# Performance work log

Measured on AMD Instinct MI355X. Metric: run time of the kernel, lower is better.

## Reference

```python
import jax, jax.numpy as jnp
import numpy as np

B, V, C, D = 32, 64, 32, 256
VOCAB = 20000
NUM_T = 1000


def _run_lstm(x, Wih, Whh, b):
    # x: [T, B, H_in]; torch-style single-layer LSTM with zero initial state
    T, Bb, _ = x.shape
    H = Whh.shape[1]
    def step(carry, xt):
        h, c = carry
        z = xt @ Wih.T + h @ Whh.T + b
        i, f, g, o = jnp.split(z, 4, axis=-1)
        c = jax.nn.sigmoid(f) * c + jax.nn.sigmoid(i) * jnp.tanh(g)
        h = jax.nn.sigmoid(o) * jnp.tanh(c)
        return (h, c), h
    h0 = jnp.zeros((Bb, H), x.dtype)
    _, ys = jax.lax.scan(step, (h0, h0), x)
    return ys


def _forward(input_seqs, masks, lengths, seq_time_step, code_masks, emb, WQ1, WK1,
             decay, initial, lstm_Wih, lstm_Whh, lstm_b, hs_Wih, hs_Whh, hs_b,
             whk_W, whk_b, w1_W, w1_b, w2_W, w2_b, fuse_W, fuse_b, lab_W, lab_b,
             betas, Wdiff, diffusion_time_t, normal_noise):
    Bb, Vv, Cc = input_seqs.shape
    tok = input_seqs.reshape(-1, Cc)                      # [B*V, C]
    x = emb[tok]                                          # [B*V, C, D]
    q = x @ WQ1.T
    k = x @ WK1.T
    dp = jnp.einsum('bcd,bed->bce', q, k)                 # [B*V, C, C]
    cm = code_masks.reshape(-1, Cc)
    dp = dp - cm[:, None, :] - cm[:, :, None]
    sp = jax.nn.softmax(dp / jnp.sqrt(jnp.float32(D)), axis=-1)
    femb = jnp.einsum('bce,bed->bcd', sp, x)              # attended code embeddings
    femb = ((cm - 1e20) / -1e20)[:, :, None] * femb       # zero out padded codes
    dec = decay[tok][..., None]                           # [B*V, C, 1]
    ini = initial[tok][..., None]
    t = seq_time_step.reshape(-1)[:, None, None]          # [B*V, 1, 1]
    gate = jax.nn.sigmoid(dec * t + ini)                  # time-decay gate
    vv = jnp.einsum('bcx,bcd->bd', gate, femb)            # [B*V, D] visit vector
    vv = vv.reshape(Bb, Vv, -1).transpose(1, 0, 2)        # [V, B, D]

    lstm_out = _run_lstm(vv, lstm_Wih, lstm_Whh, lstm_b)  # [V, B, D]
    t_lstm = lstm_out.transpose(1, 0, 2)                  # [B, V, D]
    hiddenstate = _run_lstm(lstm_out, hs_Wih, hs_Whh, hs_b).transpose(1, 0, 2)

    # Vectorized form of the original per-step python loop.
    # NOTE: the original always uses e_k = t_lstm_out[:, 0:1, :] (step 0) -- kept faithfully.
    e_k = t_lstm[:, 0:1, :]                               # [B, 1, D]
    whp = hiddenstate[:, :-1, :] @ whk_W.T + whk_b        # [B, V-1, D]
    cat = jnp.concatenate([jnp.broadcast_to(e_k, whp.shape), whp], axis=-1)
    attn = jax.nn.softmax(jnp.tanh(cat @ w1_W.T + w1_b) @ w2_W.T + w2_b, axis=-1)
    rest = e_k * attn[..., 0:1] + whp * attn[..., 1:2]
    aligned = jnp.concatenate([e_k, rest], axis=1)        # [B, V, D]

    alpha = jnp.cumprod(1.0 - betas)[diffusion_time_t][:, None, None]
    noisy = aligned * jnp.sqrt(alpha) + normal_noise * jnp.sqrt(1.0 - alpha)
    predicted_noise = noisy @ Wdiff                       # surrogate for UNetModel (source not provided)
    gen = aligned + (normal_noise - predicted_noise)

    fused = jnp.concatenate([t_lstm, gen], axis=-1) @ fuse_W.T + fuse_b   # [B, V, D]
    mask_final = (jnp.arange(Vv)[None, :] == (lengths - 1)[:, None]).astype(fused.dtype)
    final = (fused * mask_final[:, :, None]).sum(axis=1)  # select last valid visit
    return final @ lab_W.T + lab_b                        # [B, 2]


def setup_inputs() -> dict:
    key = jax.random.key(0)
    ks = jax.random.split(key, 20)
    s = 0.05
    n = lambda i, shp: jax.random.normal(ks[i], shp, jnp.float32) * s
    emb = jax.random.normal(ks[0], (VOCAB + 1, D), jnp.float32) * 0.02
    emb = emb.at[VOCAB].set(0.0)  # padding_idx row
    return {
        'input_seqs': jax.random.randint(ks[1], (B, V, C), 0, VOCAB),
        'masks': jnp.zeros((B, V), jnp.float32),
        'lengths': jax.random.randint(ks[2], (B,), 1, V + 1),
        'seq_time_step': jax.random.uniform(ks[3], (B, V), jnp.float32),
        'code_masks': jnp.zeros((B, V, C), jnp.float32),
        'emb': emb,
        'WQ1': n(4, (D, D)), 'WK1': n(5, (D, D)),
        'decay': jnp.full((VOCAB + 1,), -0.1, jnp.float32),
        'initial': jnp.full((VOCAB + 1,), 1.0, jnp.float32),
        'lstm_Wih': n(6, (4 * D, D)), 'lstm_Whh': n(7, (4 * D, D)),
        'lstm_b': jnp.zeros((4 * D,), jnp.float32),
        'hs_Wih': n(8, (4 * D, D)), 'hs_Whh': n(9, (4 * D, D)),
        'hs_b': jnp.zeros((4 * D,), jnp.float32),
        'whk_W': n(10, (D, D)), 'whk_b': jnp.zeros((D,), jnp.float32),
        'w1_W': n(11, (64, 2 * D)), 'w1_b': jnp.zeros((64,), jnp.float32),
        'w2_W': n(12, (2, 64)), 'w2_b': jnp.zeros((2,), jnp.float32),
        'fuse_W': n(13, (D, 2 * D)), 'fuse_b': jnp.zeros((D,), jnp.float32),
        'lab_W': n(14, (2, D)), 'lab_b': jnp.zeros((2,), jnp.float32),
        'betas': jnp.linspace(1e-4, 0.02, NUM_T, dtype=jnp.float32),
        'Wdiff': n(15, (D, D)),
        'diffusion_time_t': jax.random.randint(ks[16], (B,), 0, NUM_T),
        'normal_noise': jax.random.normal(ks[17], (B, V, D), jnp.float32),
    }


def reference(input_seqs, masks, lengths, seq_time_step, code_masks, emb, WQ1, WK1,
              decay, initial, lstm_Wih, lstm_Whh, lstm_b, hs_Wih, hs_Whh, hs_b,
              whk_W, whk_b, w1_W, w1_b, w2_W, w2_b, fuse_W, fuse_b, lab_W, lab_b,
              betas, Wdiff, diffusion_time_t, normal_noise):
    return _forward(input_seqs, masks, lengths, seq_time_step, code_masks, emb, WQ1, WK1,
                    decay, initial, lstm_Wih, lstm_Whh, lstm_b, hs_Wih, hs_Whh, hs_b,
                    whk_W, whk_b, w1_W, w1_b, w2_W, w2_b, fuse_W, fuse_b, lab_W, lab_b,
                    betas, Wdiff, diffusion_time_t, normal_noise)
```

## Files before the change

### kernel.cpp

```cpp
#include <hip/hip_runtime.h>
#include <hip/hip_bf16.h>
#include <cmath>

typedef __attribute__((ext_vector_type(8))) short bf16x8;
typedef __attribute__((ext_vector_type(4))) float f32x4;
typedef __attribute__((ext_vector_type(4))) int i32x4;
typedef __attribute__((ext_vector_type(2))) unsigned int u32x2;

__device__ __forceinline__ float bf2f(unsigned short u) {
    unsigned int x = ((unsigned int)u) << 16;
    return __builtin_bit_cast(float, x);
}
__device__ __forceinline__ unsigned short f2bf(float f) {
    unsigned int x = __builtin_bit_cast(unsigned int, f);
    unsigned int lsb = (x >> 16) & 1u;
    x += 0x7fffu + lsb;
    return (unsigned short)(x >> 16);
}
__device__ __forceinline__ float sigm(float z) {
    return 1.f / (1.f + __expf(-z));
}
__device__ __forceinline__ float rcpf(float x) { return __builtin_amdgcn_rcpf(x); }
__device__ __forceinline__ float sigm_f(float z) { return rcpf(1.f + __expf(-z)); }
__device__ __forceinline__ float tanh_f(float z) { return 1.f - 2.f * rcpf(1.f + __expf(2.f * z)); }

__device__ __forceinline__ long ldg_sc8l(const void* p) {
    long r;
    asm volatile("global_load_dwordx2 %0, %1, off sc1" : "=v"(r) : "v"(p) : "memory");
    return r;
}
__device__ __forceinline__ u32x2 ldg_sc_u2(const void* p) {
    u32x2 r;
    asm volatile("global_load_dwordx2 %0, %1, off sc1" : "=v"(r) : "v"(p) : "memory");
    return r;
}
__device__ __forceinline__ void stg_sc_u2(void* p, u32x2 v) {
    asm volatile("global_store_dwordx2 %0, %1, off sc1" :: "v"(p), "v"(v) : "memory");
}

__global__ void __launch_bounds__(256) pack_all(
    const float* __restrict__ Whh1, const float* __restrict__ Wih2,
    const float* __restrict__ Whh2, const float* __restrict__ Wih1,
    const float* __restrict__ WQ1, const float* __restrict__ WK1,
    const float* __restrict__ betas, const int* __restrict__ dift,
    const float* __restrict__ whk_W, const float* __restrict__ fuse_W,
    const float* __restrict__ w1_W,
    long* __restrict__ Wq, float* __restrict__ cs,
    unsigned short* __restrict__ W1h, unsigned short* __restrict__ M_pk,
    float* __restrict__ alpha, int* __restrict__ flags,
    float* __restrict__ whkT, float* __restrict__ fuseT,
    float* __restrict__ w1T) {
    int blk = blockIdx.x, tid = threadIdx.x;
    if (blk < 384) {
        int R = blk * 8 + (tid >> 5);
        int mat = R >> 10;
        int n = R & 1023;
        int t32 = tid & 31;
        const float* src = (mat == 0) ? Whh1 : (mat == 1 ? Wih2 : Whh2);
        const float* rp = src + (size_t)n * 256 + t32 * 8;
        float v[8];
        float mx = 0.f;
        for (int j = 0; j < 8; ++j) { v[j] = rp[j]; mx = fmaxf(mx, fabsf(v[j])); }
        for (int m = 1; m <= 16; m <<= 1) mx = fmaxf(mx, __shfl_xor(mx, m));
        float inv = mx > 0.f ? 127.f / mx : 0.f;
        unsigned int lo = 0, hi = 0;
        for (int j = 0; j < 4; ++j) {
            int iv = __float2int_rn(v[j] * inv);
            lo |= ((unsigned int)(unsigned char)(signed char)iv) << (8 * j);
            int iv2 = __float2int_rn(v[4 + j] * inv);
            hi |= ((unsigned int)(unsigned char)(signed char)iv2) << (8 * j);
        }
        int g = n >> 8, rem = n & 255;
        int w8 = rem >> 5, dt = (rem >> 4) & 1, cc = rem & 15;
        int t8 = g * 2 + dt;
        int kb = t32 >> 2, q = t32 & 3;
        unsigned int* dst = (unsigned int*)Wq +
            ((size_t)((mat * 512 + w8 * 64 + t8 * 8 + kb) * 64) + q * 16 + cc) * 2;
        dst[0] = lo;
        dst[1] = hi;
        if (t32 == 0) cs[mat * 1024 + n] = mx / 16129.f;
    } else if (blk < 512) {
        int cch = (blk - 384) * 256 + tid;
        int nt = cch >> 9;
        int r = cch & 511;
        int kb = r >> 6;
        int lane = r & 63;
        int grow = nt * 16 + (lane & 15);
        int k0 = kb * 32 + (lane >> 4) * 8;
        const float* sp = Wih1 + (size_t)grow * 256 + k0;
        bf16x8 hi;
        for (int j = 0; j < 8; ++j) hi[j] = (short)f2bf(sp[j]);
        *reinterpret_cast<bf16x8*>(W1h + (size_t)cch * 8) = hi;
    } else if (blk == 512) {
        if (tid < 32) {
            int tb = dift[tid];
            float p = 1.f;
            for (int i = 0; i <= tb; ++i) p *= (1.f - betas[i]);
            alpha[tid] = p;
        }
    } else if (blk == 513) {
        for (int i = tid; i < 4096; i += 256) flags[i] = 0;
    } else if (blk < 578) {
        int gid = (blk - 514) * 256 + tid;
        for (int i = 0; i < 4; ++i) {
            int e = gid + i * 16384;
            int k = e >> 8, dd = e & 255;
            whkT[e] = whk_W[(size_t)dd * 256 + k];
        }
    } else if (blk < 706) {
        int gid = (blk - 578) * 256 + tid;
        for (int i = 0; i < 4; ++i) {
            int e = gid + i * 32768;
            int k = e >> 8, dd = e & 255;
            fuseT[e] = fuse_W[(size_t)dd * 512 + k];
        }
    } else if (blk < 738) {
        int gid = (blk - 706) * 256 + tid;
        for (int i = 0; i < 4; ++i) {
            int e = gid + i * 8192;
            int k = e >> 6, j = e & 63;
            w1T[e] = w1_W[(size_t)j * 512 + k];
        }
    } else {
        __shared__ unsigned short As[256][32];
        __shared__ unsigned short Bs[256][32];
        int bx = blk - 738;
        int e0 = (bx >> 3) << 5;
        int f0 = (bx & 7) << 5;
        int col = tid & 31, rr = tid >> 5;
        for (int rep = 0; rep < 32; ++rep) {
            int d = rep * 8 + rr;
            As[d][col] = f2bf(WQ1[d * 256 + e0 + col]);
            Bs[d][col] = f2bf(WK1[d * 256 + f0 + col]);
        }
        __syncthreads();
        int el = tid & 31;
        int fl0 = tid >> 5;
        for (int i = 0; i < 4; ++i) {
            int fl = fl0 + 8 * i;
            float acc = 0.f;
            for (int d = 0; d < 256; ++d)
                acc += bf2f(As[d][el]) * bf2f(Bs[d][fl]);
            int e = e0 + el, f = f0 + fl;
            int kb = e >> 5, r = (e >> 3) & 3, j = e & 7;
            int nb = f >> 4;
            int lane = (r << 4) | (f & 15);
            M_pk[(((nb * 8 + kb) * 64) + lane) * 8 + j] = f2bf(acc);
        }
    }
}

__global__ void __launch_bounds__(256) eprep(const float* __restrict__ emb,
                                             const unsigned short* __restrict__ M_pk,
                                             unsigned short* __restrict__ Ep) {
    __shared__ __align__(16) unsigned short x_bf[32 * 256];
    int v0 = blockIdx.x * 32;
    int tid = threadIdx.x;
    for (int it = 0; it < 8; ++it) {
        int fidx = it * 256 + tid;
        int cc = fidx >> 6;
        int f4 = fidx & 63;
        int row = v0 + cc;
        float4 vx = make_float4(0.f, 0.f, 0.f, 0.f);
        if (row < 20001)
            vx = *(reinterpret_cast<const float4*>(emb + (size_t)row * 256) + f4);
        int colx = f4 * 4;
        ushort4 w;
        w.x = f2bf(vx.x); w.y = f2bf(vx.y); w.z = f2bf(vx.z); w.w = f2bf(vx.w);
        *reinterpret_cast<ushort4*>(&x_bf[cc * 256 + (colx ^ ((cc & 7) << 3))]) = w;
    }
    __syncthreads();
    int wv = tid >> 6, lane = tid & 63, lr = lane & 15, lk = lane >> 4;
    f32x4 acc[2][4];
    for (int a = 0; a < 2; ++a)
        for (int n = 0; n < 4; ++n) acc[a][n] = (f32x4){0.f, 0.f, 0.f, 0.f};
    for (int kb = 0; kb < 8; ++kb) {
        bf16x8 afr[2];
        for (int mb = 0; mb < 2; ++mb) {
            int row = mb * 16 + lr;
            int colx = kb * 32 + lk * 8;
            afr[mb] = *reinterpret_cast<const bf16x8*>(&x_bf[row * 256 + (colx ^ ((row & 7) << 3))]);
        }
        for (int nbi = 0; nbi < 4; ++nbi) {
            int nb = wv * 4 + nbi;
            bf16x8 bfr = *reinterpret_cast<const bf16x8*>(M_pk + (((nb * 8 + kb) * 64) + lane) * 8);
            acc[0][nbi] = __builtin_amdgcn_mfma_f32_16x16x32_bf16(afr[0], bfr, acc[0][nbi], 0, 0, 0);
            acc[1][nbi] = __builtin_amdgcn_mfma_f32_16x16x32_bf16(afr[1], bfr, acc[1][nbi], 0, 0, 0);
        }
    }
    for (int mb = 0; mb < 2; ++mb)
        for (int nbi = 0; nbi < 4; ++nbi)
            for (int r = 0; r < 4; ++r) {
                int row = mb * 16 + lk * 4 + r;
                int col = wv * 64 + nbi * 16 + lr;
                if (v0 + row < 20001)
                    Ep[(size_t)(v0 + row) * 256 + col] = f2bf(acc[mb][nbi][r]);
            }
}

__global__ void __launch_bounds__(256) attn_bags(
    const int* __restrict__ seqs, const float* __restrict__ tstep,
    const float* __restrict__ cmask, const float* __restrict__ emb,
    const float* __restrict__ decay, const float* __restrict__ initial,
    const unsigned short* __restrict__ Ep, float* __restrict__ vv) {
    __shared__ __align__(16) unsigned short x_bf[32 * 256];
    __shared__ __align__(16) unsigned short t1_bf[32 * 256];
    __shared__ float dp_f[32 * 33];
    __shared__ float gate_sh[32];
    __shared__ float cm_sh[32];
    __shared__ int tok_sh[32];
    __shared__ float w_sh[32];

    int bag = blockIdx.x;
    int tid = threadIdx.x;

    if (tid < 32) {
        int tok = seqs[bag * 32 + tid];
        tok_sh[tid] = tok;
        float cm = cmask[bag * 32 + tid];
        cm_sh[tid] = cm;
        float tt = tstep[bag];
        float g = sigm(decay[tok] * tt + initial[tok]);
        g *= (cm - 1e20f) / (-1e20f);
        gate_sh[tid] = g;
    }
    __syncthreads();

    for (int it = 0; it < 8; ++it) {
        int fidx = it * 256 + tid;
        int c = fidx >> 6;
        int f4 = fidx & 63;
        const float4* src = reinterpret_cast<const float4*>(emb + (size_t)tok_sh[c] * 256) + f4;
        float4 vx = *src;
        int colx = f4 * 4;
        int eidx = c * 256 + (colx ^ ((c & 7) << 3));
        ushort4 w;
        w.x = f2bf(vx.x); w.y = f2bf(vx.y); w.z = f2bf(vx.z); w.w = f2bf(vx.w);
        *reinterpret_cast<ushort4*>(&x_bf[eidx]) = w;
    }
    for (int it = 0; it < 4; ++it) {
        int idx = it * 256 + tid;
        int cc = idx >> 5;
        int colx = (idx & 31) * 8;
        bf16x8 e = *reinterpret_cast<const bf16x8*>(Ep + (size_t)tok_sh[cc] * 256 + colx);
        *reinterpret_cast<bf16x8*>(&t1_bf[cc * 256 + (colx ^ ((cc & 7) << 3))]) = e;
    }
    __syncthreads();

    int wv = tid >> 6;
    int lane = tid & 63;
    int lr = lane & 15;
    int lk = lane >> 4;

    {
        int mb = wv >> 1, nb2 = wv & 1;
        f32x4 dacc = (f32x4){0.f, 0.f, 0.f, 0.f};
        for (int kb = 0; kb < 8; ++kb) {
            int cola = kb * 32 + lk * 8;
            int rowa = mb * 16 + lr;
            bf16x8 afr = *reinterpret_cast<const bf16x8*>(&t1_bf[rowa * 256 + (cola ^ ((rowa & 7) << 3))]);
            int rowb = nb2 * 16 + lr;
            bf16x8 bfr = *reinterpret_cast<const bf16x8*>(&x_bf[rowb * 256 + (cola ^ ((rowb & 7) << 3))]);
            dacc = __builtin_amdgcn_mfma_f32_16x16x32_bf16(afr, bfr, dacc, 0, 0, 0);
        }
        for (int r = 0; r < 4; ++r) {
            int c = mb * 16 + lk * 4 + r;
            int e = nb2 * 16 + lr;
            dp_f[c * 33 + e] = dacc[r];
        }
    }
    __syncthreads();

    if (tid < 32) {
        int c = tid;
        float cmc = cm_sh[c];
        float lg[32];
        float mx = -1e30f;
        for (int e = 0; e < 32; ++e) {
            float l = (dp_f[c * 33 + e] - cmc - cm_sh[e]) * 0.0625f;
            lg[e] = l;
            mx = fmaxf(mx, l);
        }
        float s = 0.f;
        for (int e = 0; e < 32; ++e) { float ex = __expf(lg[e] - mx); lg[e] = ex; s += ex; }
        float inv = 1.f / s;
        for (int e = 0; e < 32; ++e) dp_f[c * 33 + e] = lg[e] * inv;
    }
    __syncthreads();
    if (tid < 32) {
        int e = tid;
        float a2 = 0.f;
        for (int c = 0; c < 32; ++c) a2 += gate_sh[c] * dp_f[c * 33 + e];
        w_sh[e] = a2;
    }
    __syncthreads();

    float accv = 0.f;
    int d = tid;
    for (int e = 0; e < 32; ++e)
        accv += w_sh[e] * bf2f(x_bf[e * 256 + (d ^ ((e & 7) << 3))]);
    vv[(size_t)bag * 256 + d] = accv;
}

__global__ void __launch_bounds__(256) x1_mfma(const float* __restrict__ vv,
                                               const unsigned short* __restrict__ W1h,
                                               const float* __restrict__ lstm_b,
                                               unsigned short* __restrict__ X1bf) {
    __shared__ __align__(16) unsigned short xs[32 * 256];
    int blk = blockIdx.x;
    int rb = blk >> 3, gb = blk & 7;
    int tid = threadIdx.x;
    for (int it = 0; it < 8; ++it) {
        int idx = it * 256 + tid;
        int row = idx >> 6, f4 = idx & 63;
        float4 v = *reinterpret_cast<const float4*>(vv + (size_t)(rb * 32 + row) * 256 + f4 * 4);
        ushort4 w;
        w.x = f2bf(v.x); w.y = f2bf(v.y); w.z = f2bf(v.z); w.w = f2bf(v.w);
        *reinterpret_cast<ushort4*>(&xs[row * 256 + ((f4 * 4) ^ ((row & 7) << 3))]) = w;
    }
    __syncthreads();
    int wv = tid >> 6, lane = tid & 63, cl = lane & 15, kh = lane >> 4;
    f32x4 acc[2][2];
    for (int n = 0; n < 2; ++n) {
        int nt = gb * 8 + wv * 2 + n;
        float bz = lstm_b[nt * 16 + cl];
        acc[n][0] = (f32x4){bz, bz, bz, bz};
        acc[n][1] = (f32x4){bz, bz, bz, bz};
    }
    #pragma unroll
    for (int kb = 0; kb < 8; ++kb) {
        int k = kb * 32 + kh * 8;
        bf16x8 a0 = *reinterpret_cast<const bf16x8*>(&xs[cl * 256 + (k ^ ((cl & 7) << 3))]);
        bf16x8 a1 = *reinterpret_cast<const bf16x8*>(&xs[(16 + cl) * 256 + (k ^ (((16 + cl) & 7) << 3))]);
        for (int n = 0; n < 2; ++n) {
            int nt = gb * 8 + wv * 2 + n;
            size_t o = ((size_t)(nt * 8 + kb) * 64 + lane) * 8;
            bf16x8 bh = *reinterpret_cast<const bf16x8*>(W1h + o);
            acc[n][0] = __builtin_amdgcn_mfma_f32_16x16x32_bf16(a0, bh, acc[n][0], 0, 0, 0);
            acc[n][1] = __builtin_amdgcn_mfma_f32_16x16x32_bf16(a1, bh, acc[n][1], 0, 0, 0);
        }
    }
    for (int n = 0; n < 2; ++n) {
        int nt = gb * 8 + wv * 2 + n;
        int g = nt * 16 + cl;
        int dX = g & 255, gt = g >> 8;
        for (int mt = 0; mt < 2; ++mt)
            for (int r = 0; r < 4; ++r) {
                int row = rb * 32 + mt * 16 + kh * 4 + r;
                int b = row >> 6, t = row & 63;
                X1bf[((size_t)t * 32 + b) * 1024 + dX * 4 + gt] = f2bf(acc[n][mt][r]);
            }
    }
}

__global__ void __launch_bounds__(512, 2) lstm_persist(
    const long* __restrict__ Wq, const float* __restrict__ cs,
    const unsigned short* __restrict__ X1bf, const float* __restrict__ hs_b,
    unsigned short* __restrict__ h1bf, unsigned short* __restrict__ h2bf,
    signed char* h1q, unsigned short* p1, int* flags) {
    int role = blockIdx.x;
    int half = role & 1;
    int kind = role >> 1;
    int tid = threadIdx.x;
    int w = tid >> 6, lane = tid & 63, c = lane & 15, q = lane >> 4;

    long wt[64];
    #pragma unroll
    for (int t8 = 0; t8 < 8; ++t8)
        #pragma unroll
        for (int kb = 0; kb < 8; ++kb)
            wt[t8 * 8 + kb] = Wq[(size_t)((kind * 512 + w * 64 + t8 * 8 + kb) * 64) + lane];
    float csv[8];
    #pragma unroll
    for (int t8 = 0; t8 < 8; ++t8) {
        int g = t8 >> 1, dt = t8 & 1;
        csv[t8] = cs[kind * 1024 + g * 256 + w * 32 + dt * 16 + c];
    }

    if (kind == 0) {
        __shared__ signed char hq[2][16][272];
        float cstate[8] = {0.f, 0.f, 0.f, 0.f, 0.f, 0.f, 0.f, 0.f};
        int B0 = half * 16 + q * 4;
        int dbase = w * 32;
        for (int t = 0; t < 64; ++t) {
            ushort4 xv[8];
            #pragma unroll
            for (int dt = 0; dt < 2; ++dt)
                #pragma unroll
                for (int r = 0; r < 4; ++r)
                    xv[dt * 4 + r] = *reinterpret_cast<const ushort4*>(
                        X1bf + ((size_t)(t * 32 + B0 + r) * 1024 + (dbase + dt * 16 + c) * 4));
            i32x4 acc[8];
            #pragma unroll
            for (int i = 0; i < 8; ++i) acc[i] = (i32x4){0, 0, 0, 0};
            if (t > 0) {
                int pb = (t - 1) & 1;
                long a[8];
                #pragma unroll
                for (int kb = 0; kb < 8; ++kb)
                    a[kb] = *reinterpret_cast<const long*>(&hq[pb][c][kb * 32 + q * 8]);
                #pragma unroll
                for (int t8 = 0; t8 < 8; ++t8)
                    #pragma unroll
                    for (int kb = 0; kb < 8; ++kb)
                        acc[t8] = __builtin_amdgcn_mfma_i32_16x16x32_i8(
                            a[kb], wt[t8 * 8 + kb], acc[t8], 0, 0, 0);
            }
            float hnv[8];
            unsigned int hvb[8];
            #pragma unroll
            for (int dt = 0; dt < 2; ++dt)
                #pragma unroll
                for (int r = 0; r < 4; ++r) {
                    int idx = dt * 4 + r;
                    ushort4 x = xv[idx];
                    float zi = (float)acc[0 + dt][r] * csv[0 + dt] + bf2f(x.x);
                    float zf = (float)acc[2 + dt][r] * csv[2 + dt] + bf2f(x.y);
                    float zg = (float)acc[4 + dt][r] * csv[4 + dt] + bf2f(x.z);
                    float zo = (float)acc[6 + dt][r] * csv[6 + dt] + bf2f(x.w);
                    float cn = sigm_f(zf) * cstate[idx] + sigm_f(zi) * tanh_f(zg);
                    float hn = sigm_f(zo) * tanh_f(cn);
                    cstate[idx] = cn;
                    hnv[idx] = hn;
                    int hv = __float2int_rn(hn * 127.f);
                    hq[t & 1][q * 4 + r][dbase + dt * 16 + c] = (signed char)hv;
                    hvb[idx] = (unsigned int)(unsigned char)(signed char)hv;
                }
            #pragma unroll
            for (int dt = 0; dt < 2; ++dt)
                #pragma unroll
                for (int r = 0; r < 4; ++r) {
                    unsigned int b = hvb[dt * 4 + r];
                    unsigned int p = (unsigned int)__shfl_xor((int)b, 1);
                    unsigned int pair = (c & 1) ? (p | (b << 8)) : (b | (p << 8));
                    unsigned int pq = (unsigned int)__shfl_xor((int)pair, 2);
                    unsigned int quad = (c & 2) ? (pq | (pair << 16)) : (pair | (pq << 16));
                    unsigned int oh = (unsigned int)__shfl_xor((int)quad, 4);
                    if ((c & 7) == 0) {
                        u32x2 v8;
                        v8.x = quad; v8.y = oh;
                        stg_sc_u2(h1q + (size_t)(t * 32 + B0 + r) * 256 + dbase + dt * 16 + c, v8);
                    }
                }
            #pragma unroll
            for (int dt = 0; dt < 2; ++dt)
                #pragma unroll
                for (int r = 0; r < 4; ++r) {
                    unsigned int ph = f2bf(hnv[dt * 4 + r]);
                    unsigned int pp = (unsigned int)__shfl_xor((int)ph, 1);
                    if (!(c & 1))
                        *reinterpret_cast<unsigned int*>(
                            h1bf + (size_t)(t * 32 + B0 + r) * 256 + dbase + dt * 16 + c) =
                            ph | (pp << 16);
                }
            __syncthreads();
            if (tid == 0)
                __hip_atomic_store(flags + (t * 2 + half) * 16, 1,
                                   __ATOMIC_RELAXED, __HIP_MEMORY_SCOPE_AGENT);
        }
    } else if (kind == 1) {
        for (int s2 = 0; s2 < 64; s2 += 2) {
            const int* fp = flags + ((s2 + 1) * 2 + half) * 16;
            while (__hip_atomic_load(fp, __ATOMIC_RELAXED, __HIP_MEMORY_SCOPE_AGENT) == 0)
                __builtin_amdgcn_s_sleep(1);
            __builtin_amdgcn_sched_barrier(0);
            const signed char* hb0 = h1q + (size_t)(s2 * 32 + half * 16) * 256;
            const signed char* hb1 = h1q + (size_t)((s2 + 1) * 32 + half * 16) * 256;
            long a[8], b[8];
            #pragma unroll
            for (int kb = 0; kb < 8; ++kb) {
                a[kb] = ldg_sc8l(hb0 + c * 256 + kb * 32 + q * 8);
                b[kb] = ldg_sc8l(hb1 + c * 256 + kb * 32 + q * 8);
            }
            asm volatile("s_waitcnt vmcnt(0)" ::: "memory");
            __builtin_amdgcn_sched_barrier(0);
            #pragma unroll
            for (int step = 0; step < 2; ++step) {
                int s = s2 + step;
                i32x4 acc[8];
                #pragma unroll
                for (int i = 0; i < 8; ++i) acc[i] = (i32x4){0, 0, 0, 0};
                #pragma unroll
                for (int t8 = 0; t8 < 8; ++t8)
                    #pragma unroll
                    for (int kb = 0; kb < 8; ++kb)
                        acc[t8] = __builtin_amdgcn_mfma_i32_16x16x32_i8(
                            step ? b[kb] : a[kb], wt[t8 * 8 + kb], acc[t8], 0, 0, 0);
                #pragma unroll
                for (int t8 = 0; t8 < 8; ++t8) {
                    int g = t8 >> 1, dt = t8 & 1;
                    int n = g * 256 + w * 32 + dt * 16 + c;
                    u32x2 pv;
                    pv.x = (unsigned int)f2bf((float)acc[t8][0] * csv[t8]) |
                           ((unsigned int)f2bf((float)acc[t8][1] * csv[t8]) << 16);
                    pv.y = (unsigned int)f2bf((float)acc[t8][2] * csv[t8]) |
                           ((unsigned int)f2bf((float)acc[t8][3] * csv[t8]) << 16);
                    stg_sc_u2(p1 + ((size_t)(s * 2 + half) * 1024 + n) * 16 + q * 4, pv);
                }
            }
            __syncthreads();
            if (tid == 0)
                __hip_atomic_store(flags + 2048 + ((s2 >> 1) * 2 + half) * 16, 1,
                                   __ATOMIC_RELAXED, __HIP_MEMORY_SCOPE_AGENT);
        }
    } else {
        __shared__ signed char hq2[2][16][272];
        float cstate[8] = {0.f, 0.f, 0.f, 0.f, 0.f, 0.f, 0.f, 0.f};
        float bias[8];
        #pragma unroll
        for (int t8 = 0; t8 < 8; ++t8) {
            int g = t8 >> 1, dt = t8 & 1;
            bias[t8] = hs_b[g * 256 + w * 32 + dt * 16 + c];
        }
        int B0 = half * 16 + q * 4;
        int dbase = w * 32;
        for (int s = 0; s < 64; ++s) {
            if ((s & 1) == 0) {
                const int* fp = flags + 2048 + ((s >> 1) * 2 + half) * 16;
                while (__hip_atomic_load(fp, __ATOMIC_RELAXED, __HIP_MEMORY_SCOPE_AGENT) == 0)
                    __builtin_amdgcn_s_sleep(1);
                __builtin_amdgcn_sched_barrier(0);
            }
            u32x2 pv[8];
            #pragma unroll
            for (int t8 = 0; t8 < 8; ++t8) {
                int g = t8 >> 1, dt = t8 & 1;
                int n = g * 256 + w * 32 + dt * 16 + c;
                pv[t8] = ldg_sc_u2(p1 + ((size_t)(s * 2 + half) * 1024 + n) * 16 + q * 4);
            }
            i32x4 acc[8];
            #pragma unroll
            for (int i = 0; i < 8; ++i) acc[i] = (i32x4){0, 0, 0, 0};
            if (s > 0) {
                int pb = (s - 1) & 1;
                long a[8];
                #pragma unroll
                for (int kb = 0; kb < 8; ++kb)
                    a[kb] = *reinterpret_cast<const long*>(&hq2[pb][c][kb * 32 + q * 8]);
                asm volatile("s_waitcnt vmcnt(0)" ::: "memory");
                __builtin_amdgcn_sched_barrier(0);
                #pragma unroll
                for (int t8 = 0; t8 < 8; ++t8)
                    #pragma unroll
                    for (int kb = 0; kb < 8; ++kb)
                        acc[t8] = __builtin_amdgcn_mfma_i32_16x16x32_i8(
                            a[kb], wt[t8 * 8 + kb], acc[t8], 0, 0, 0);
            } else {
                asm volatile("s_waitcnt vmcnt(0)" ::: "memory");
                __builtin_amdgcn_sched_barrier(0);
            }
            float hnv[8];
            #pragma unroll
            for (int dt = 0; dt < 2; ++dt)
                #pragma unroll
                for (int r = 0; r < 4; ++r) {
                    int idx = dt * 4 + r;
                    float p_i = bf2f((unsigned short)((r < 2 ? pv[0 + dt].x : pv[0 + dt].y) >> ((r & 1) * 16)));
                    float p_f = bf2f((unsigned short)((r < 2 ? pv[2 + dt].x : pv[2 + dt].y) >> ((r & 1) * 16)));
                    float p_g = bf2f((unsigned short)((r < 2 ? pv[4 + dt].x : pv[4 + dt].y) >> ((r & 1) * 16)));
                    float p_o = bf2f((unsigned short)((r < 2 ? pv[6 + dt].x : pv[6 + dt].y) >> ((r & 1) * 16)));
                    float zi = (float)acc[0 + dt][r] * csv[0 + dt] + p_i + bias[0 + dt];
                    float zf = (float)acc[2 + dt][r] * csv[2 + dt] + p_f + bias[2 + dt];
                    float zg = (float)acc[4 + dt][r] * csv[4 + dt] + p_g + bias[4 + dt];
                    float zo = (float)acc[6 + dt][r] * csv[6 + dt] + p_o + bias[6 + dt];
                    float cn = sigm_f(zf) * cstate[idx] + sigm_f(zi) * tanh_f(zg);
                    float hn = sigm_f(zo) * tanh_f(cn);
                    cstate[idx] = cn;
                    hnv[idx] = hn;
                    hq2[s & 1][q * 4 + r][dbase + dt * 16 + c] = (signed char)__float2int_rn(hn * 127.f);
                }
            #pragma unroll
            for (int dt = 0; dt < 2; ++dt)
                #pragma unroll
                for (int r = 0; r < 4; ++r) {
                    unsigned int ph = f2bf(hnv[dt * 4 + r]);
                    unsigned int pp = (unsigned int)__shfl_xor((int)ph, 1);
                    if (!(c & 1))
                        *reinterpret_cast<unsigned int*>(
                            h2bf + (size_t)(s * 32 + B0 + r) * 256 + dbase + dt * 16 + c) =
                            ph | (pp << 16);
                }
            __syncthreads();
        }
    }
}

__global__ void __launch_bounds__(256) tail_k(
    const int* __restrict__ lengths,
    const unsigned short* __restrict__ h1, const unsigned short* __restrict__ h2,
    const float* __restrict__ whkT, const float* __restrict__ whk_b,
    const float* __restrict__ w1T, const float* __restrict__ w1_b,
    const float* __restrict__ w2_W, const float* __restrict__ w2_b,
    const float* __restrict__ fuseT, const float* __restrict__ fuse_b,
    const float* __restrict__ lab_W, const float* __restrict__ lab_b,
    const float* __restrict__ Wdiff, const float* __restrict__ alpha,
    const float* __restrict__ noise, float* __restrict__ out) {
    __shared__ float ek[256], tv[256], hs[256], whp[256], a1s[64];
    __shared__ float noisy_s[256], fin[512], fused_s[256], attn_s[2];
    int b = blockIdx.x, tid = threadIdx.x;
    int vstar = lengths[b] - 1;
    {
        ek[tid] = bf2f(h1[(size_t)b * 256 + tid]);
        tv[tid] = bf2f(h1[((size_t)vstar * 32 + b) * 256 + tid]);
        if (vstar > 0)
            hs[tid] = bf2f(h2[((size_t)(vstar - 1) * 32 + b) * 256 + tid]);
    }
    __syncthreads();

    float aligned;
    if (vstar > 0) {
        float s0 = 0.f, s1 = 0.f, s2 = 0.f, s3 = 0.f;
        for (int k = 0; k < 256; k += 4) {
            s0 += whkT[(k + 0) * 256 + tid] * hs[k + 0];
            s1 += whkT[(k + 1) * 256 + tid] * hs[k + 1];
            s2 += whkT[(k + 2) * 256 + tid] * hs[k + 2];
            s3 += whkT[(k + 3) * 256 + tid] * hs[k + 3];
        }
        whp[tid] = whk_b[tid] + s0 + s1 + s2 + s3;
        __syncthreads();
        if (tid < 64) {
            float a0 = 0.f, a1 = 0.f, a2 = 0.f, a3 = 0.f;
            for (int k = 0; k < 256; k += 4) {
                a0 += w1T[(k + 0) * 64 + tid] * ek[k + 0];
                a1 += w1T[(k + 1) * 64 + tid] * ek[k + 1];
                a2 += w1T[(k + 2) * 64 + tid] * ek[k + 2];
                a3 += w1T[(k + 3) * 64 + tid] * ek[k + 3];
            }
            for (int k = 0; k < 256; k += 4) {
                a0 += w1T[(256 + k + 0) * 64 + tid] * whp[k + 0];
                a1 += w1T[(256 + k + 1) * 64 + tid] * whp[k + 1];
                a2 += w1T[(256 + k + 2) * 64 + tid] * whp[k + 2];
                a3 += w1T[(256 + k + 3) * 64 + tid] * whp[k + 3];
            }
            a1s[tid] = tanhf(w1_b[tid] + a0 + a1 + a2 + a3);
        }
        __syncthreads();
        if (tid < 2) {
            float a3 = w2_b[tid];
            const float* wr2 = w2_W + tid * 64;
            for (int k = 0; k < 64; ++k) a3 += wr2[k] * a1s[k];
            attn_s[tid] = a3;
        }
        __syncthreads();
        float m = fmaxf(attn_s[0], attn_s[1]);
        float e0 = __expf(attn_s[0] - m), e1 = __expf(attn_s[1] - m);
        float inv = 1.f / (e0 + e1);
        aligned = ek[tid] * (e0 * inv) + whp[tid] * (e1 * inv);
    } else {
        aligned = ek[tid];
    }

    float al = alpha[b];
    float sa = sqrtf(al), sb = sqrtf(1.f - al);
    float nz = noise[((size_t)b * 64 + vstar) * 256 + tid];
    noisy_s[tid] = aligned * sa + nz * sb;
    __syncthreads();
    {
        float p0 = 0.f, p1v = 0.f, p2 = 0.f, p3 = 0.f;
        for (int k = 0; k < 256; k += 4) {
            p0 += noisy_s[k + 0] * Wdiff[(size_t)(k + 0) * 256 + tid];
            p1v += noisy_s[k + 1] * Wdiff[(size_t)(k + 1) * 256 + tid];
            p2 += noisy_s[k + 2] * Wdiff[(size_t)(k + 2) * 256 + tid];
            p3 += noisy_s[k + 3] * Wdiff[(size_t)(k + 3) * 256 + tid];
        }
        float gen = aligned + nz - (p0 + p1v + p2 + p3);
        fin[tid] = tv[tid];
        fin[256 + tid] = gen;
    }
    __syncthreads();
    {
        float f0 = 0.f, f1 = 0.f, f2 = 0.f, f3 = 0.f;
        for (int k = 0; k < 512; k += 4) {
            f0 += fuseT[(k + 0) * 256 + tid] * fin[k + 0];
            f1 += fuseT[(k + 1) * 256 + tid] * fin[k + 1];
            f2 += fuseT[(k + 2) * 256 + tid] * fin[k + 2];
            f3 += fuseT[(k + 3) * 256 + tid] * fin[k + 3];
        }
        fused_s[tid] = fuse_b[tid] + f0 + f1 + f2 + f3;
    }
    __syncthreads();
    if (tid < 2) {
        float o = lab_b[tid];
        const float* lw = lab_W + tid * 256;
        for (int k = 0; k < 256; ++k) o += lw[k] * fused_s[k];
        out[b * 2 + tid] = o;
    }
}

extern "C" void kernel_launch(void* const* d_in, const int* in_sizes, int n_in,
                              void* d_out, int out_size, void* d_ws, size_t ws_size,
                              hipStream_t stream) {
    const int*   seqs    = (const int*)  d_in[0];
    const int*   lengths = (const int*)  d_in[2];
    const float* tstep   = (const float*)d_in[3];
    const float* cmask   = (const float*)d_in[4];
    const float* emb     = (const float*)d_in[5];
    const float* WQ1     = (const float*)d_in[6];
    const float* WK1     = (const float*)d_in[7];
    const float* decay   = (const float*)d_in[8];
    const float* initial = (const float*)d_in[9];
    const float* Wih1    = (const float*)d_in[10];
    const float* Whh1    = (const float*)d_in[11];
    const float* lstm_b  = (const float*)d_in[12];
    const float* Wih2    = (const float*)d_in[13];
    const float* Whh2    = (const float*)d_in[14];
    const float* hs_b    = (const float*)d_in[15];
    const float* whk_W   = (const float*)d_in[16];
    const float* whk_b   = (const float*)d_in[17];
    const float* w1_W    = (const float*)d_in[18];
    const float* w1_b    = (const float*)d_in[19];
    const float* w2_W    = (const float*)d_in[20];
    const float* w2_b    = (const float*)d_in[21];
    const float* fuse_W  = (const float*)d_in[22];
    const float* fuse_b  = (const float*)d_in[23];
    const float* lab_W   = (const float*)d_in[24];
    const float* lab_b   = (const float*)d_in[25];
    const float* betas   = (const float*)d_in[26];
    const float* Wdiff   = (const float*)d_in[27];
    const int*   dift    = (const int*)  d_in[28];
    const float* noise   = (const float*)d_in[29];
    float* out = (float*)d_out;

    float* ws = (float*)d_ws;
    size_t off = 0;
    auto alloc = [&](size_t nfloats) { size_t r = off; off += (nfloats + 63) & ~(size_t)63; return r; };
    unsigned short* M_pk  = (unsigned short*)(ws + alloc(32768));
    float*          alpha = ws + alloc(64);
    float*          cs    = ws + alloc(3072);
    int*            flags = (int*)(ws + alloc(4096));
    float*          vv    = ws + alloc(524288);
    unsigned short* X1bf  = (unsigned short*)(ws + alloc(1048576));
    unsigned short* h1bf  = (unsigned short*)(ws + alloc(262144));
    unsigned short* h2bf  = (unsigned short*)(ws + alloc(262144));
    unsigned short* p1    = (unsigned short*)(ws + alloc(1048576));
    long*           Wq    = (long*)(ws + alloc(196608));
    unsigned short* W1h   = (unsigned short*)(ws + alloc(131072));
    float*          whkT  = ws + alloc(65536);
    float*          fuseT = ws + alloc(131072);
    float*          w1T   = ws + alloc(32768);
    signed char*    h1q   = (signed char*)(ws + alloc(131072));
    unsigned short* Ep    = (unsigned short*)(ws + alloc(2560128));

    pack_all<<<802, 256, 0, stream>>>(Whh1, Wih2, Whh2, Wih1, WQ1, WK1, betas, dift,
                                      whk_W, fuse_W, w1_W,
                                      Wq, cs, W1h, M_pk, alpha, flags,
                                      whkT, fuseT, w1T);
    eprep<<<626, 256, 0, stream>>>(emb, M_pk, Ep);
    attn_bags<<<2048, 256, 0, stream>>>(seqs, tstep, cmask, emb, decay, initial, Ep, vv);
    x1_mfma<<<512, 256, 0, stream>>>(vv, W1h, lstm_b, X1bf);
    lstm_persist<<<6, 512, 0, stream>>>(Wq, cs, X1bf, hs_b, h1bf, h2bf, h1q, p1, flags);
    tail_k<<<32, 256, 0, stream>>>(lengths, h1bf, h2bf, whkT, whk_b,
                                   w1T, w1_b, w2_W, w2_b, fuseT, fuse_b,
                                   lab_W, lab_b, Wdiff, alpha, noise, out);
}
```

Baseline: 373.4 us.

## Split LSTM recurrence over 16 waves per block and pipeline projection per step

The persistent LSTM kernel now launches 1024 threads (16 waves) per role block instead of 512, so each wave owns 16 hidden units and 32 MFMAs per step instead of 32 units and 64. This halves per-wave register-resident weights and the serial MFMA chain on the recurrent critical path. The projection role also changes from batching two timesteps per flag wait to signalling every step, which lets the second LSTM start sooner. The cost is more flag polling traffic and more waves contending for the same CU's MFMA units.

Result: slower. 441.1 us (+18.2%).

```diff
diff --git a/kernel.cpp b/kernel.cpp
--- a/kernel.cpp
+++ b/kernel.cpp
@@ -353,7 +353,7 @@
     }
 }
 
-__global__ void __launch_bounds__(512, 2) lstm_persist(
+__global__ void __launch_bounds__(1024, 4) lstm_persist(
     const long* __restrict__ Wq, const float* __restrict__ cs,
     const unsigned short* __restrict__ X1bf, const float* __restrict__ hs_b,
     unsigned short* __restrict__ h1bf, unsigned short* __restrict__ h2bf,
@@ -362,37 +362,33 @@
     int half = role & 1;
     int kind = role >> 1;
     int tid = threadIdx.x;
-    int w = tid >> 6, lane = tid & 63, c = lane & 15, q = lane >> 4;
-
-    long wt[64];
+    int w = tid >> 6;
+    int lane = tid & 63, c = lane & 15, q = lane >> 4;
+    int d = w * 16 + c;
+
+    long wt[4][8];
     #pragma unroll
-    for (int t8 = 0; t8 < 8; ++t8)
+    for (int g = 0; g < 4; ++g)
         #pragma unroll
         for (int kb = 0; kb < 8; ++kb)
-            wt[t8 * 8 + kb] = Wq[(size_t)((kind * 512 + w * 64 + t8 * 8 + kb) * 64) + lane];
-    float csv[8];
+            wt[g][kb] = Wq[(size_t)((kind * 512 + (w >> 1) * 64 + (g * 2 + (w & 1)) * 8 + kb) * 64) + lane];
+    float csv[4];
     #pragma unroll
-    for (int t8 = 0; t8 < 8; ++t8) {
-        int g = t8 >> 1, dt = t8 & 1;
-        csv[t8] = cs[kind * 1024 + g * 256 + w * 32 + dt * 16 + c];
-    }
+    for (int g = 0; g < 4; ++g) csv[g] = cs[kind * 1024 + g * 256 + d];
 
     if (kind == 0) {
         __shared__ signed char hq[2][16][272];
-        float cstate[8] = {0.f, 0.f, 0.f, 0.f, 0.f, 0.f, 0.f, 0.f};
+        float cstate[4] = {0.f, 0.f, 0.f, 0.f};
         int B0 = half * 16 + q * 4;
-        int dbase = w * 32;
         for (int t = 0; t < 64; ++t) {
-            ushort4 xv[8];
-            #pragma unroll
-            for (int dt = 0; dt < 2; ++dt)
-                #pragma unroll
-                for (int r = 0; r < 4; ++r)
-                    xv[dt * 4 + r] = *reinterpret_cast<const ushort4*>(
-                        X1bf + ((size_t)(t * 32 + B0 + r) * 1024 + (dbase + dt * 16 + c) * 4));
-            i32x4 acc[8];
-            #pragma unroll
-            for (int i = 0; i < 8; ++i) acc[i] = (i32x4){0, 0, 0, 0};
+            ushort4 xv[4];
+            #pragma unroll
+            for (int r = 0; r < 4; ++r)
+                xv[r] = *reinterpret_cast<const ushort4*>(
+                    X1bf + ((size_t)(t * 32 + B0 + r) * 1024 + d * 4));
+            i32x4 acc[4];
+            #pragma unroll
+            for (int g = 0; g < 4; ++g) acc[g] = (i32x4){0, 0, 0, 0};
             if (t > 0) {
                 int pb = (t - 1) & 1;
                 long a[8];
@@ -400,137 +396,112 @@
                 for (int kb = 0; kb < 8; ++kb)
                     a[kb] = *reinterpret_cast<const long*>(&hq[pb][c][kb * 32 + q * 8]);
                 #pragma unroll
-                for (int t8 = 0; t8 < 8; ++t8)
+                for (int g = 0; g < 4; ++g)
                     #pragma unroll
                     for (int kb = 0; kb < 8; ++kb)
-                        acc[t8] = __builtin_amdgcn_mfma_i32_16x16x32_i8(
-                            a[kb], wt[t8 * 8 + kb], acc[t8], 0, 0, 0);
-            }
-            float hnv[8];
-            unsigned int hvb[8];
-            #pragma unroll
-            for (int dt = 0; dt < 2; ++dt)
-                #pragma unroll
-                for (int r = 0; r < 4; ++r) {
-                    int idx = dt * 4 + r;
-                    ushort4 x = xv[idx];
-                    float zi = (float)acc[0 + dt][r] * csv[0 + dt] + bf2f(x.x);
-                    float zf = (float)acc[2 + dt][r] * csv[2 + dt] + bf2f(x.y);
-                    float zg = (float)acc[4 + dt][r] * csv[4 + dt] + bf2f(x.z);
-                    float zo = (float)acc[6 + dt][r] * csv[6 + dt] + bf2f(x.w);
-                    float cn = sigm_f(zf) * cstate[idx] + sigm_f(zi) * tanh_f(zg);
-                    float hn = sigm_f(zo) * tanh_f(cn);
-                    cstate[idx] = cn;
-                    hnv[idx] = hn;
-                    int hv = __float2int_rn(hn * 127.f);
-                    hq[t & 1][q * 4 + r][dbase + dt * 16 + c] = (signed char)hv;
-                    hvb[idx] = (unsigned int)(unsigned char)(signed char)hv;
+                        acc[g] = __builtin_amdgcn_mfma_i32_16x16x32_i8(
+                            a[kb], wt[g][kb], acc[g], 0, 0, 0);
+            }
+            float hnv[4];
+            unsigned int hvb[4];
+            #pragma unroll
+            for (int r = 0; r < 4; ++r) {
+                ushort4 x = xv[r];
+                float zi = (float)acc[0][r] * csv[0] + bf2f(x.x);
+                float zf = (float)acc[1][r] * csv[1] + bf2f(x.y);
+                float zg = (float)acc[2][r] * csv[2] + bf2f(x.z);
+                float zo = (float)acc[3][r] * csv[3] + bf2f(x.w);
+                float cn = sigm_f(zf) * cstate[r] + sigm_f(zi) * tanh_f(zg);
+                float hn = sigm_f(zo) * tanh_f(cn);
+                cstate[r] = cn;
+                hnv[r] = hn;
+                int hv = __float2int_rn(hn * 127.f);
+                hq[t & 1][q * 4 + r][d] = (signed char)hv;
+                hvb[r] = (unsigned int)(unsigned char)(signed char)hv;
+            }
+            #pragma unroll
+            for (int r = 0; r < 4; ++r) {
+                unsigned int b = hvb[r];
+                unsigned int p = (unsigned int)__shfl_xor((int)b, 1);
+                unsigned int pair = (c & 1) ? (p | (b << 8)) : (b | (p << 8));
+                unsigned int pq = (unsigned int)__shfl_xor((int)pair, 2);
+                unsigned int quad = (c & 2) ? (pq | (pair << 16)) : (pair | (pq << 16));
+                unsigned int oh = (unsigned int)__shfl_xor((int)quad, 4);
+                if ((c & 7) == 0) {
+                    u32x2 v8;
+                    v8.x = quad; v8.y = oh;
+                    stg_sc_u2(h1q + (size_t)(t * 32 + B0 + r) * 256 + d, v8);
                 }
-            #pragma unroll
-            for (int dt = 0; dt < 2; ++dt)
-                #pragma unroll
-                for (int r = 0; r < 4; ++r) {
-                    unsigned int b = hvb[dt * 4 + r];
-                    unsigned int p = (unsigned int)__shfl_xor((int)b, 1);
-                    unsigned int pair = (c & 1) ? (p | (b << 8)) : (b | (p << 8));
-                    unsigned int pq = (unsigned int)__shfl_xor((int)pair, 2);
-                    unsigned int quad = (c & 2) ? (pq | (pair << 16)) : (pair | (pq << 16));
-                    unsigned int oh = (unsigned int)__shfl_xor((int)quad, 4);
-                    if ((c & 7) == 0) {
-                        u32x2 v8;
-                        v8.x = quad; v8.y = oh;
-                        stg_sc_u2(h1q + (size_t)(t * 32 + B0 + r) * 256 + dbase + dt * 16 + c, v8);
-                    }
-                }
-            #pragma unroll
-            for (int dt = 0; dt < 2; ++dt)
-                #pragma unroll
-                for (int r = 0; r < 4; ++r) {
-                    unsigned int ph = f2bf(hnv[dt * 4 + r]);
-                    unsigned int pp = (unsigned int)__shfl_xor((int)ph, 1);
-                    if (!(c & 1))
-                        *reinterpret_cast<unsigned int*>(
-                            h1bf + (size_t)(t * 32 + B0 + r) * 256 + dbase + dt * 16 + c) =
-                            ph | (pp << 16);
-                }
+            }
+            #pragma unroll
+            for (int r = 0; r < 4; ++r) {
+                unsigned int ph = f2bf(hnv[r]);
+                unsigned int pp = (unsigned int)__shfl_xor((int)ph, 1);
+                if (!(c & 1))
+                    *reinterpret_cast<unsigned int*>(
+                        h1bf + (size_t)(t * 32 + B0 + r) * 256 + d) = ph | (pp << 16);
+            }
             __syncthreads();
             if (tid == 0)
                 __hip_atomic_store(flags + (t * 2 + half) * 16, 1,
                                    __ATOMIC_RELAXED, __HIP_MEMORY_SCOPE_AGENT);
         }
     } else if (kind == 1) {
-        for (int s2 = 0; s2 < 64; s2 += 2) {
-            const int* fp = flags + ((s2 + 1) * 2 + half) * 16;
+        for (int s = 0; s < 64; ++s) {
+            const int* fp = flags + (s * 2 + half) * 16;
             while (__hip_atomic_load(fp, __ATOMIC_RELAXED, __HIP_MEMORY_SCOPE_AGENT) == 0)
                 __builtin_amdgcn_s_sleep(1);
             __builtin_amdgcn_sched_barrier(0);
-            const signed char* hb0 = h1q + (size_t)(s2 * 32 + half * 16) * 256;
-            const signed char* hb1 = h1q + (size_t)((s2 + 1) * 32 + half * 16) * 256;
-            long a[8], b[8];
-            #pragma unroll
-            for (int kb = 0; kb < 8; ++kb) {
-                a[kb] = ldg_sc8l(hb0 + c * 256 + kb * 32 + q * 8);
-                b[kb] = ldg_sc8l(hb1 + c * 256 + kb * 32 + q * 8);
-            }
+            const signed char* hb = h1q + (size_t)(s * 32 + half * 16) * 256;
+            long a[8];
+            #pragma unroll
+            for (int kb = 0; kb < 8; ++kb)
+                a[kb] = ldg_sc8l(hb + c * 256 + kb * 32 + q * 8);
             asm volatile("s_waitcnt vmcnt(0)" ::: "memory");
             __builtin_amdgcn_sched_barrier(0);
-            #pragma unroll
-            for (int step = 0; step < 2; ++step) {
-                int s = s2 + step;
-                i32x4 acc[8];
+            i32x4 acc[4];
+            #pragma unroll
+            for (int g = 0; g < 4; ++g) acc[g] = (i32x4){0, 0, 0, 0};
+            #pragma unroll
+            for (int g = 0; g < 4; ++g)
                 #pragma unroll
-                for (int i = 0; i < 8; ++i) acc[i] = (i32x4){0, 0, 0, 0};
-                #pragma unroll
-                for (int t8 = 0; t8 < 8; ++t8)
-                    #pragma unroll
-                    for (int kb = 0; kb < 8; ++kb)
-                        acc[t8] = __builtin_amdgcn_mfma_i32_16x16x32_i8(
-                            step ? b[kb] : a[kb], wt[t8 * 8 + kb], acc[t8], 0, 0, 0);
-                #pragma unroll
-                for (int t8 = 0; t8 < 8; ++t8) {
-                    int g = t8 >> 1, dt = t8 & 1;
-                    int n = g * 256 + w * 32 + dt * 16 + c;
-                    u32x2 pv;
-                    pv.x = (unsigned int)f2bf((float)acc[t8][0] * csv[t8]) |
-                           ((unsigned int)f2bf((float)acc[t8][1] * csv[t8]) << 16);
-                    pv.y = (unsigned int)f2bf((float)acc[t8][2] * csv[t8]) |
-                           ((unsigned int)f2bf((float)acc[t8][3] * csv[t8]) << 16);
-                    stg_sc_u2(p1 + ((size_t)(s * 2 + half) * 1024 + n) * 16 + q * 4, pv);
-                }
+                for (int kb = 0; kb < 8; ++kb)
+                    acc[g] = __builtin_amdgcn_mfma_i32_16x16x32_i8(
+                        a[kb], wt[g][kb], acc[g], 0, 0, 0);
+            #pragma unroll
+            for (int g = 0; g < 4; ++g) {
+                int n = g * 256 + d;
+                u32x2 pv;
+                pv.x = (unsigned int)f2bf((float)acc[g][0] * csv[g]) |
+                       ((unsigned int)f2bf((float)acc[g][1] * csv[g]) << 16);
+                pv.y = (unsigned int)f2bf((float)acc[g][2] * csv[g]) |
+                       ((unsigned int)f2bf((float)acc[g][3] * csv[g]) << 16);
+                stg_sc_u2(p1 + ((size_t)(s * 2 + half) * 1024 + n) * 16 + q * 4, pv);
             }
             __syncthreads();
             if (tid == 0)
-                __hip_atomic_store(flags + 2048 + ((s2 >> 1) * 2 + half) * 16, 1,
+                __hip_atomic_store(flags + 2048 + (s * 2 + half) * 16, 1,
                                    __ATOMIC_RELAXED, __HIP_MEMORY_SCOPE_AGENT);
         }
     } else {
         __shared__ signed char hq2[2][16][272];
-        float cstate[8] = {0.f, 0.f, 0.f, 0.f, 0.f, 0.f, 0.f, 0.f};
-        float bias[8];
+        float cstate[4] = {0.f, 0.f, 0.f, 0.f};
+        float bias[4];
         #pragma unroll
-        for (int t8 = 0; t8 < 8; ++t8) {
-            int g = t8 >> 1, dt = t8 & 1;
-            bias[t8] = hs_b[g * 256 + w * 32 + dt * 16 + c];
-        }
+        for (int g = 0; g < 4; ++g) bias[g] = hs_b[g * 256 + d];
         int B0 = half * 16 + q * 4;
-        int dbase = w * 32;
         for (int s = 0; s < 64; ++s) {
-            if ((s & 1) == 0) {
-                const int* fp = flags + 2048 + ((s >> 1) * 2 + half) * 16;
-                while (__hip_atomic_load(fp, __ATOMIC_RELAXED, __HIP_MEMORY_SCOPE_AGENT) == 0)
-                    __builtin_amdgcn_s_sleep(1);
-                __builtin_amdgcn_sched_barrier(0);
-            }
-            u32x2 pv[8];
-            #pragma unroll
-            for (int t8 = 0; t8 < 8; ++t8) {
-                int g = t8 >> 1, dt = t8 & 1;
-                int n = g * 256 + w * 32 + dt * 16 + c;
-                pv[t8] = ldg_sc_u2(p1 + ((size_t)(s * 2 + half) * 1024 + n) * 16 + q * 4);
-            }
-            i32x4 acc[8];
-            #pragma unroll
-            for (int i = 0; i < 8; ++i) acc[i] = (i32x4){0, 0, 0, 0};
+            const int* fp = flags + 2048 + (s * 2 + half) * 16;
+            while (__hip_atomic_load(fp, __ATOMIC_RELAXED, __HIP_MEMORY_SCOPE_AGENT) == 0)
+                __builtin_amdgcn_s_sleep(1);
+            __builtin_amdgcn_sched_barrier(0);
+            u32x2 pv[4];
+            #pragma unroll
+            for (int g = 0; g < 4; ++g)
+                pv[g] = ldg_sc_u2(p1 + ((size_t)(s * 2 + half) * 1024 + g * 256 + d) * 16 + q * 4);
+            i32x4 acc[4];
+            #pragma unroll
+            for (int g = 0; g < 4; ++g) acc[g] = (i32x4){0, 0, 0, 0};
             if (s > 0) {
                 int pb = (s - 1) & 1;
                 long a[8];
@@ -540,46 +511,40 @@
                 asm volatile("s_waitcnt vmcnt(0)" ::: "memory");
                 __builtin_amdgcn_sched_barrier(0);
                 #pragma unroll
-                for (int t8 = 0; t8 < 8; ++t8)
+                for (int g = 0; g < 4; ++g)
                     #pragma unroll
                     for (int kb = 0; kb < 8; ++kb)
-                        acc[t8] = __builtin_amdgcn_mfma_i32_16x16x32_i8(
-                            a[kb], wt[t8 * 8 + kb], acc[t8], 0, 0, 0);
+                        acc[g] = __builtin_amdgcn_mfma_i32_16x16x32_i8(
+                            a[kb], wt[g][kb], acc[g], 0, 0, 0);
             } else {
                 asm volatile("s_waitcnt vmcnt(0)" ::: "memory");
                 __builtin_amdgcn_sched_barrier(0);
             }
-            float hnv[8];
-            #pragma unroll
-            for (int dt = 0; dt < 2; ++dt)
-                #pragma unroll
-                for (int r = 0; r < 4; ++r) {
-                    int idx = dt * 4 + r;
-                    float p_i = bf2f((unsigned short)((r < 2 ? pv[0 + dt].x : pv[0 + dt].y) >> ((r & 1) * 16)));
-                    float p_f = bf2f((unsigned short)((r < 2 ? pv[2 + dt].x : pv[2 + dt].y) >> ((r & 1) * 16)));
-                    float p_g = bf2f((unsigned short)((r < 2 ? pv[4 + dt].x : pv[4 + dt].y) >> ((r & 1) * 16)));
-                    float p_o = bf2f((unsigned short)((r < 2 ? pv[6 + dt].x : pv[6 + dt].y) >> ((r & 1) * 16)));
-                    float zi = (float)acc[0 + dt][r] * csv[0 + dt] + p_i + bias[0 + dt];
-                    float zf = (float)acc[2 + dt][r] * csv[2 + dt] + p_f + bias[2 + dt];
-                    float zg = (float)acc[4 + dt][r] * csv[4 + dt] + p_g + bias[4 + dt];
-                    float zo = (float)acc[6 + dt][r] * csv[6 + dt] + p_o + bias[6 + dt];
-                    float cn = sigm_f(zf) * cstate[idx] + sigm_f(zi) * tanh_f(zg);
-                    float hn = sigm_f(zo) * tanh_f(cn);
-                    cstate[idx] = cn;
-                    hnv[idx] = hn;
-                    hq2[s & 1][q * 4 + r][dbase + dt * 16 + c] = (signed char)__float2int_rn(hn * 127.f);
-                }
-            #pragma unroll
-            for (int dt = 0; dt < 2; ++dt)
-                #pragma unroll
-                for (int r = 0; r < 4; ++r) {
-                    unsigned int ph = f2bf(hnv[dt * 4 + r]);
-                    unsigned int pp = (unsigned int)__shfl_xor((int)ph, 1);
-                    if (!(c & 1))
-                        *reinterpret_cast<unsigned int*>(
-                            h2bf + (size_t)(s * 32 + B0 + r) * 256 + dbase + dt * 16 + c) =
-                            ph | (pp << 16);
-                }
+            float hnv[4];
+            #pragma unroll
+            for (int r = 0; r < 4; ++r) {
+                float p_i = bf2f((unsigned short)((r < 2 ? pv[0].x : pv[0].y) >> ((r & 1) * 16)));
+                float p_f = bf2f((unsigned short)((r < 2 ? pv[1].x : pv[1].y) >> ((r & 1) * 16)));
+                float p_g = bf2f((unsigned short)((r < 2 ? pv[2].x : pv[2].y) >> ((r & 1) * 16)));
+                float p_o = bf2f((unsigned short)((r < 2 ? pv[3].x : pv[3].y) >> ((r & 1) * 16)));
+                float zi = (float)acc[0][r] * csv[0] + p_i + bias[0];
+                float zf = (float)acc[1][r] * csv[1] + p_f + bias[1];
+                float zg = (float)acc[2][r] * csv[2] + p_g + bias[2];
+                float zo = (float)acc[3][r] * csv[3] + p_o + bias[3];
+                float cn = sigm_f(zf) * cstate[r] + sigm_f(zi) * tanh_f(zg);
+                float hn = sigm_f(zo) * tanh_f(cn);
+                cstate[r] = cn;
+                hnv[r] = hn;
+                hq2[s & 1][q * 4 + r][d] = (signed char)__float2int_rn(hn * 127.f);
+            }
+            #pragma unroll
+            for (int r = 0; r < 4; ++r) {
+                unsigned int ph = f2bf(hnv[r]);
+                unsigned int pp = (unsigned int)__shfl_xor((int)ph, 1);
+                if (!(c & 1))
+                    *reinterpret_cast<unsigned int*>(
+                        h2bf + (size_t)(s * 32 + B0 + r) * 256 + d) = ph | (pp << 16);
+            }
             __syncthreads();
         }
     }
@@ -748,7 +713,7 @@
     eprep<<<626, 256, 0, stream>>>(emb, M_pk, Ep);
     attn_bags<<<2048, 256, 0, stream>>>(seqs, tstep, cmask, emb, decay, initial, Ep, vv);
     x1_mfma<<<512, 256, 0, stream>>>(vv, W1h, lstm_b, X1bf);
-    lstm_persist<<<6, 512, 0, stream>>>(Wq, cs, X1bf, hs_b, h1bf, h2bf, h1q, p1, flags);
+    lstm_persist<<<6, 1024, 0, stream>>>(Wq, cs, X1bf, hs_b, h1bf, h2bf, h1q, p1, flags);
     tail_k<<<32, 256, 0, stream>>>(lengths, h1bf, h2bf, whkT, whk_b,
                                    w1T, w1_b, w2_W, w2_b, fuseT, fuse_b,
                                    lab_W, lab_b, Wdiff, alpha, noise, out);
```
